# Kernel tuning notes

Measured on AMD Instinct MI355X. Metric: run time of the kernel, lower is better.

Reference implementation:

```python
import jax, jax.numpy as jnp
import numpy as np

N_NODES = 50000
N_EDGES = 800000
IN_FEAT = 64
HIDDEN = 128
NUM_LAYERS = 3


def setup_inputs() -> dict:
    key = jax.random.key(0)
    ks = jax.random.split(key, 8)
    x = jax.random.normal(ks[0], (N_NODES, IN_FEAT), dtype=jnp.float32)
    edge_index = jax.random.randint(ks[1], (2, N_EDGES), 0, N_NODES, dtype=jnp.int64)
    s_in = 1.0 / np.sqrt(IN_FEAT)
    s_h = 1.0 / np.sqrt(HIDDEN)
    W_in = jax.random.uniform(ks[2], (IN_FEAT, HIDDEN), jnp.float32, -s_in, s_in)
    b_in = jax.random.uniform(ks[3], (HIDDEN,), jnp.float32, -s_in, s_in)
    W_self = jax.random.uniform(ks[4], (NUM_LAYERS, HIDDEN, HIDDEN), jnp.float32, -s_h, s_h)
    b_self = jax.random.uniform(ks[5], (NUM_LAYERS, HIDDEN), jnp.float32, -s_h, s_h)
    W_nbr = jax.random.uniform(ks[6], (NUM_LAYERS, HIDDEN, HIDDEN), jnp.float32, -s_h, s_h)
    return {"x": x, "edge_index": edge_index, "W_in": W_in, "b_in": b_in,
            "W_self": W_self, "b_self": b_self, "W_nbr": W_nbr}


def reference(x, edge_index, W_in, b_in, W_self, b_self, W_nbr):
    # input projection: h [N, HIDDEN]
    h = x @ W_in + b_in
    src = edge_index[0]
    dst = edge_index[1]
    n = h.shape[0]
    ones = jnp.ones((dst.shape[0], 1), dtype=h.dtype)
    # scatter-mean denominator is grad-constant; compute once
    cnt = jax.ops.segment_sum(ones, dst, num_segments=n)
    cnt = jnp.maximum(cnt, 1.0)
    for l in range(W_self.shape[0]):
        msg = h[src] @ W_nbr[l]                               # [E, HIDDEN]
        agg = jax.ops.segment_sum(msg, dst, num_segments=n) / cnt  # scatter-mean
        h = jax.nn.elu(h @ W_self[l] + b_self[l] + agg)
    return h
```

## Files before the change

kernel.cpp:

```cpp
#include <hip/hip_runtime.h>
#include <cstdint>

#define HIDDEN 128

typedef unsigned short u16;
using frag_t  = __attribute__((ext_vector_type(8))) short;
using f32x4_t = __attribute__((ext_vector_type(4))) float;

__device__ __forceinline__ float bf2f(u16 u) {
    union { unsigned int i; float f; } c;
    c.i = ((unsigned int)u) << 16;
    return c.f;
}
__device__ __forceinline__ u16 f2bf(float f) {
    unsigned int u = __float_as_uint(f);
    unsigned int r = (u + 0x7fffu + ((u >> 16) & 1u)) >> 16;
    return (u16)r;
}

__device__ __forceinline__ size_t fmaj(int row, int col, int KF) {
    int T = row >> 4, m = row & 15;
    int f = col >> 5, q = (col & 31) >> 3, j = col & 7;
    return ((size_t)(T * KF + f) * 64 + q * 16 + m) * 8 + j;
}


__global__ void k_hist(const int* __restrict__ ei, int E, int* __restrict__ deg, int npr) {
    int r  = blockIdx.x & 7;
    int lo = r * npr, hi = lo + npr;
    int nb = gridDim.x >> 3;
    int bi = blockIdx.x >> 3;
    int tid = bi * blockDim.x + threadIdx.x;
    int stride = nb * blockDim.x;
    if ((E & 3) == 0) {
        const int4* d4 = (const int4*)(ei + E);
        int nch = E >> 2;
        for (int c = tid; c < nch; c += stride) {
            int4 d = d4[c];
            if (d.x >= lo && d.x < hi) atomicAdd(&deg[d.x], 1);
            if (d.y >= lo && d.y < hi) atomicAdd(&deg[d.y], 1);
            if (d.z >= lo && d.z < hi) atomicAdd(&deg[d.z], 1);
            if (d.w >= lo && d.w < hi) atomicAdd(&deg[d.w], 1);
        }
    } else {
        for (int e = tid; e < E; e += stride) {
            int d = ei[E + e];
            if (d >= lo && d < hi) atomicAdd(&deg[d], 1);
        }
    }
}

__global__ void k_scan1(const int* __restrict__ deg, int* __restrict__ rowp,
                        int* __restrict__ bsums, int n) {
    __shared__ int sh[1024];
    int t = threadIdx.x;
    int base = blockIdx.x * 1024;
    int v = (base + t < n) ? deg[base + t] : 0;
    sh[t] = v;
    __syncthreads();
    for (int off = 1; off < 1024; off <<= 1) {
        int x = sh[t];
        int y = (t >= off) ? sh[t - off] : 0;
        __syncthreads();
        sh[t] = x + y;
        __syncthreads();
    }
    if (base + t < n) rowp[base + t + 1] = sh[t];
    if (t == 1023) bsums[blockIdx.x] = sh[1023];
}

__global__ void k_scan2(int* __restrict__ bsums, int nb) {
    if (threadIdx.x == 0 && blockIdx.x == 0) {
        int run = 0;
        for (int b = 0; b < nb; ++b) { int v = bsums[b]; bsums[b] = run; run += v; }
    }
}

__global__ void k_scan3(int* __restrict__ rowp, const int* __restrict__ boffs,
                        int* __restrict__ fillp, int n) {
    int t = threadIdx.x;
    int b = blockIdx.x;
    int base = b * 1024;
    if (base + t < n) {
        int v = rowp[base + t + 1] + boffs[b];
        rowp[base + t + 1] = v;
        if (base + t + 1 < n) fillp[base + t + 1] = v;
    }
    if (b == 0 && t == 0) { rowp[0] = 0; fillp[0] = 0; }
}

__global__ void k_fill(const int* __restrict__ ei, int E,
                       int* __restrict__ fillpos, int* __restrict__ colx, int npr) {
    int r  = blockIdx.x & 7;
    int lo = r * npr, hi = lo + npr;
    int nb = gridDim.x >> 3;
    int bi = blockIdx.x >> 3;
    int tid = bi * blockDim.x + threadIdx.x;
    int stride = nb * blockDim.x;
    if ((E & 3) == 0) {
        const int4* s4 = (const int4*)ei;
        const int4* d4 = (const int4*)(ei + E);
        int nch = E >> 2;
        for (int c = tid; c < nch; c += stride) {
            int4 d = d4[c];
            bool m0 = d.x >= lo && d.x < hi;
            bool m1 = d.y >= lo && d.y < hi;
            bool m2 = d.z >= lo && d.z < hi;
            bool m3 = d.w >= lo && d.w < hi;
            if (m0 | m1 | m2 | m3) {
                int4 s = s4[c];
                if (m0) colx[atomicAdd(&fillpos[d.x], 1)] = s.x;
                if (m1) colx[atomicAdd(&fillpos[d.y], 1)] = s.y;
                if (m2) colx[atomicAdd(&fillpos[d.z], 1)] = s.z;
                if (m3) colx[atomicAdd(&fillpos[d.w], 1)] = s.w;
            }
        }
    } else {
        for (int e = tid; e < E; e += stride) {
            int d = ei[E + e];
            if (d >= lo && d < hi) colx[atomicAdd(&fillpos[d], 1)] = ei[e];
        }
    }
}


__global__ void k_prep_w(const float* __restrict__ W_in,
                         const float* __restrict__ W_self,
                         const float* __restrict__ W_nbr,
                         u16* __restrict__ WtI_hi, u16* __restrict__ WtI_lo,
                         u16* __restrict__ WtS_hi, u16* __restrict__ WtS_lo,
                         u16* __restrict__ WtN_hi, u16* __restrict__ WtN_lo,
                         int L) {
    int idx = blockIdx.x * blockDim.x + threadIdx.x;
    int nIn = 64 * 128;
    int nSq = L * 128 * 128;
    float v; u16* phi; u16* plo; int o;
    if (idx < nIn) {
        int n = idx / 64, k = idx % 64;
        v = W_in[k * 128 + n]; phi = WtI_hi; plo = WtI_lo; o = n * 64 + k;
    } else if (idx < nIn + nSq) {
        int t = idx - nIn;
        int l = t / (128 * 128), r = t % (128 * 128);
        int n = r / 128, k = r % 128;
        v = W_self[l * 128 * 128 + k * 128 + n]; phi = WtS_hi; plo = WtS_lo;
        o = l * 128 * 128 + n * 128 + k;
    } else if (idx < nIn + 2 * nSq) {
        int t = idx - nIn - nSq;
        int l = t / (128 * 128), r = t % (128 * 128);
        int n = r / 128, k = r % 128;
        v = W_nbr[l * 128 * 128 + k * 128 + n]; phi = WtN_hi; plo = WtN_lo;
        o = l * 128 * 128 + n * 128 + k;
    } else return;
    u16 hi = f2bf(v);
    phi[o] = hi;
    plo[o] = f2bf(v - bf2f(hi));
}

__global__ void k_prep_x(const float* __restrict__ x, u16* __restrict__ xf, int total) {
    int i = blockIdx.x * blockDim.x + threadIdx.x;
    int stride = gridDim.x * blockDim.x;
    for (; i < total; i += stride) {
        int row = i >> 6, col = i & 63;
        xf[fmaj(row, col, 2)] = f2bf(x[i]);
    }
}


__global__ void k_agg(const ushort4* __restrict__ hb4, const int* __restrict__ rowp,
                      const int* __restrict__ colx, u16* __restrict__ Sf, int n) {
    int g = (blockIdx.x * blockDim.x + threadIdx.x) >> 5;
    int lane = threadIdx.x & 31;
    if (g >= n) return;
    int beg = rowp[g];
    int end = rowp[g + 1];
    float4 a0 = make_float4(0.f, 0.f, 0.f, 0.f);
    float4 a1 = a0, a2 = a0, a3 = a0;
    int e = beg;
    for (; e + 7 < end; e += 8) {
        int s0 = colx[e],     s1 = colx[e + 1], s2 = colx[e + 2], s3 = colx[e + 3];
        int s4 = colx[e + 4], s5 = colx[e + 5], s6 = colx[e + 6], s7 = colx[e + 7];
        ushort4 v0 = hb4[(size_t)s0 * 32 + lane];
        ushort4 v1 = hb4[(size_t)s1 * 32 + lane];
        ushort4 v2 = hb4[(size_t)s2 * 32 + lane];
        ushort4 v3 = hb4[(size_t)s3 * 32 + lane];
        ushort4 v4 = hb4[(size_t)s4 * 32 + lane];
        ushort4 v5 = hb4[(size_t)s5 * 32 + lane];
        ushort4 v6 = hb4[(size_t)s6 * 32 + lane];
        ushort4 v7 = hb4[(size_t)s7 * 32 + lane];
        a0.x += bf2f(v0.x); a0.y += bf2f(v0.y); a0.z += bf2f(v0.z); a0.w += bf2f(v0.w);
        a1.x += bf2f(v1.x); a1.y += bf2f(v1.y); a1.z += bf2f(v1.z); a1.w += bf2f(v1.w);
        a2.x += bf2f(v2.x); a2.y += bf2f(v2.y); a2.z += bf2f(v2.z); a2.w += bf2f(v2.w);
        a3.x += bf2f(v3.x); a3.y += bf2f(v3.y); a3.z += bf2f(v3.z); a3.w += bf2f(v3.w);
        a0.x += bf2f(v4.x); a0.y += bf2f(v4.y); a0.z += bf2f(v4.z); a0.w += bf2f(v4.w);
        a1.x += bf2f(v5.x); a1.y += bf2f(v5.y); a1.z += bf2f(v5.z); a1.w += bf2f(v5.w);
        a2.x += bf2f(v6.x); a2.y += bf2f(v6.y); a2.z += bf2f(v6.z); a2.w += bf2f(v6.w);
        a3.x += bf2f(v7.x); a3.y += bf2f(v7.y); a3.z += bf2f(v7.z); a3.w += bf2f(v7.w);
    }
    for (; e + 3 < end; e += 4) {
        int s0 = colx[e], s1 = colx[e + 1], s2 = colx[e + 2], s3 = colx[e + 3];
        ushort4 v0 = hb4[(size_t)s0 * 32 + lane];
        ushort4 v1 = hb4[(size_t)s1 * 32 + lane];
        ushort4 v2 = hb4[(size_t)s2 * 32 + lane];
        ushort4 v3 = hb4[(size_t)s3 * 32 + lane];
        a0.x += bf2f(v0.x); a0.y += bf2f(v0.y); a0.z += bf2f(v0.z); a0.w += bf2f(v0.w);
        a1.x += bf2f(v1.x); a1.y += bf2f(v1.y); a1.z += bf2f(v1.z); a1.w += bf2f(v1.w);
        a2.x += bf2f(v2.x); a2.y += bf2f(v2.y); a2.z += bf2f(v2.z); a2.w += bf2f(v2.w);
        a3.x += bf2f(v3.x); a3.y += bf2f(v3.y); a3.z += bf2f(v3.z); a3.w += bf2f(v3.w);
    }
    for (; e < end; ++e) {
        int s = colx[e];
        ushort4 v = hb4[(size_t)s * 32 + lane];
        a0.x += bf2f(v.x); a0.y += bf2f(v.y); a0.z += bf2f(v.z); a0.w += bf2f(v.w);
    }
    float acc[4];
    acc[0] = (a0.x + a1.x) + (a2.x + a3.x);
    acc[1] = (a0.y + a1.y) + (a2.y + a3.y);
    acc[2] = (a0.z + a1.z) + (a2.z + a3.z);
    acc[3] = (a0.w + a1.w) + (a2.w + a3.w);
    int deg = end - beg;
    float inv = 1.0f / (float)(deg > 1 ? deg : 1);
    ushort4 ohi;
    u16* ph = &ohi.x;
#pragma unroll
    for (int c = 0; c < 4; ++c) ph[c] = f2bf(acc[c] * inv);
    int T = g >> 4, m = g & 15;
    int f = lane >> 3;
    int q = (lane & 7) >> 1;
    int jo = (lane & 1) * 4;
    *(ushort4*)&Sf[((size_t)(T * 4 + f) * 64 + q * 16 + m) * 8 + jo] = ohi;
}


template <int KF1, int KF2>
__global__ __launch_bounds__(256, 2) void k_gemm_mfma(
    const u16* __restrict__ A1f, const u16* __restrict__ A2f,
    const u16* __restrict__ B1h, const u16* __restrict__ B1l,
    const u16* __restrict__ B2h, const u16* __restrict__ B2l,
    const float* __restrict__ bias, float* __restrict__ C,
    u16* __restrict__ Hrow, u16* __restrict__ Hf,
    int M, int do_elu)
{
    constexpr int K1 = KF1 * 32;
    constexpr int K2 = KF2 * 32;
    constexpr int KF = KF1 + KF2;
    int lane = threadIdx.x & 63;
    int w    = threadIdx.x >> 6;
    int m16  = lane & 15;
    int quad = lane >> 4;
    int kq   = quad * 8;
    int ng   = (blockIdx.x >> 3) & 1;
    int mtb  = (blockIdx.x & 7) | ((blockIdx.x >> 4) << 3);
    int ncol = (ng * 4 + w) * 16 + m16;

    frag_t bh[KF], bl[KF];
    if (KF1) {
#pragma unroll
        for (int f = 0; f < KF1; ++f) {
            bh[f] = *(const frag_t*)&B1h[(size_t)ncol * K1 + f * 32 + kq];
            bl[f] = *(const frag_t*)&B1l[(size_t)ncol * K1 + f * 32 + kq];
        }
    }
    if (KF2) {
#pragma unroll
        for (int f = 0; f < KF2; ++f) {
            bh[KF1 + f] = *(const frag_t*)&B2h[(size_t)ncol * K2 + f * 32 + kq];
            bl[KF1 + f] = *(const frag_t*)&B2l[(size_t)ncol * K2 + f * 32 + kq];
        }
    }

    float bv = bias[ncol];
    int nMT  = (M + 31) >> 5;
    int step = gridDim.x >> 1;
    int fcol = ncol >> 5;
    int qcol = (ncol & 31) >> 3;
    int jcol = ncol & 7;

    for (int mt = mtb; mt < nMT; mt += step) {
        int T0 = mt * 2, T1 = T0 + 1;

        frag_t a0[KF], a1[KF];
        if (KF1) {
#pragma unroll
            for (int f = 0; f < KF1; ++f) {
                a0[f] = *(const frag_t*)&A1f[((size_t)(T0 * KF1 + f) * 64 + lane) * 8];
                a1[f] = *(const frag_t*)&A1f[((size_t)(T1 * KF1 + f) * 64 + lane) * 8];
            }
        }
        if (KF2) {
#pragma unroll
            for (int f = 0; f < KF2; ++f) {
                a0[KF1 + f] = *(const frag_t*)&A2f[((size_t)(T0 * KF2 + f) * 64 + lane) * 8];
                a1[KF1 + f] = *(const frag_t*)&A2f[((size_t)(T1 * KF2 + f) * 64 + lane) * 8];
            }
        }

        f32x4_t acc0 = (f32x4_t){0.f, 0.f, 0.f, 0.f};
        f32x4_t acc1 = (f32x4_t){0.f, 0.f, 0.f, 0.f};
#pragma unroll
        for (int f = 0; f < KF; ++f) {
            acc0 = __builtin_amdgcn_mfma_f32_16x16x32_bf16(a0[f], bh[f], acc0, 0, 0, 0);
            acc1 = __builtin_amdgcn_mfma_f32_16x16x32_bf16(a1[f], bh[f], acc1, 0, 0, 0);
            acc0 = __builtin_amdgcn_mfma_f32_16x16x32_bf16(a0[f], bl[f], acc0, 0, 0, 0);
            acc1 = __builtin_amdgcn_mfma_f32_16x16x32_bf16(a1[f], bl[f], acc1, 0, 0, 0);
        }

        int rb = mt * 32 + quad * 4;
#pragma unroll
        for (int r = 0; r < 4; ++r) {
#pragma unroll
            for (int half = 0; half < 2; ++half) {
                int row = rb + r + half * 16;
                float av = half ? acc1[r] : acc0[r];
                if (row < M) {
                    float v = av + bv;
                    if (do_elu) v = (v > 0.f) ? v : expm1f(v);
                    if (C) C[(size_t)row * HIDDEN + ncol] = v;
                    if (Hrow) {
                        u16 hv = f2bf(v);
                        Hrow[(size_t)row * HIDDEN + ncol] = hv;
                        Hf[((size_t)((row >> 4) * 4 + fcol) * 64 + qcol * 16 + (row & 15)) * 8 + jcol] = hv;
                    }
                }
            }
        }
    }
}


extern "C" void kernel_launch(void* const* d_in, const int* in_sizes, int n_in,
                              void* d_out, int out_size, void* d_ws, size_t ws_size,
                              hipStream_t stream) {
    const float* x        = (const float*)d_in[0];
    const int* ei         = (const int*)d_in[1];
    const float* W_in     = (const float*)d_in[2];
    const float* b_in     = (const float*)d_in[3];
    const float* W_self   = (const float*)d_in[4];
    const float* b_self   = (const float*)d_in[5];
    const float* W_nbr    = (const float*)d_in[6];
    float* out = (float*)d_out;

    const int IN_FEAT = 64;
    int N = in_sizes[0] / IN_FEAT;
    int E = in_sizes[1] / 2;
    int L = in_sizes[4] / (HIDDEN * HIDDEN);

    char* ws = (char*)d_ws;
    size_t off = 0;
    auto alloc = [&](size_t bytes) -> void* {
        void* p = ws + off;
        off = (off + bytes + 255) & ~(size_t)255;
        return p;
    };

    int nT = ((N + 31) / 32) * 2;

    u16* hRowA = (u16*)alloc((size_t)N * HIDDEN * 2);
    u16* hRowB = (u16*)alloc((size_t)N * HIDDEN * 2);
    u16* hfA   = (u16*)alloc((size_t)nT * 4 * 64 * 8 * 2);
    u16* hfB   = (u16*)alloc((size_t)nT * 4 * 64 * 8 * 2);
    u16* xf    = (u16*)alloc((size_t)nT * 2 * 64 * 8 * 2);
    u16* Sf    = (u16*)alloc((size_t)nT * 4 * 64 * 8 * 2);
    u16* WtI_hi = (u16*)alloc(128 * 64 * 2);
    u16* WtI_lo = (u16*)alloc(128 * 64 * 2);
    u16* WtS_hi = (u16*)alloc((size_t)L * 128 * 128 * 2);
    u16* WtS_lo = (u16*)alloc((size_t)L * 128 * 128 * 2);
    u16* WtN_hi = (u16*)alloc((size_t)L * 128 * 128 * 2);
    u16* WtN_lo = (u16*)alloc((size_t)L * 128 * 128 * 2);
    int* deg   = (int*)alloc((size_t)N * sizeof(int));
    int* rowp  = (int*)alloc((size_t)(N + 1) * sizeof(int));
    int* fillp = (int*)alloc((size_t)N * sizeof(int));
    int* colx  = (int*)alloc((size_t)E * sizeof(int));
    int* bsums = (int*)alloc(256 * sizeof(int));

    int npr = (N + 7) / 8;

    hipMemsetAsync(deg, 0, (size_t)N * sizeof(int), stream);
    k_hist<<<2048, 256, 0, stream>>>(ei, E, deg, npr);
    int nb = (N + 1023) / 1024;
    k_scan1<<<nb, 1024, 0, stream>>>(deg, rowp, bsums, N);
    k_scan2<<<1, 64, 0, stream>>>(bsums, nb);
    k_scan3<<<nb, 1024, 0, stream>>>(rowp, bsums, fillp, N);
    k_fill<<<2048, 256, 0, stream>>>(ei, E, fillp, colx, npr);

    int wtot = 64 * 128 + 2 * L * 128 * 128;
    k_prep_w<<<(wtot + 255) / 256, 256, 0, stream>>>(W_in, W_self, W_nbr,
                                                     WtI_hi, WtI_lo, WtS_hi, WtS_lo,
                                                     WtN_hi, WtN_lo, L);
    k_prep_x<<<1024, 256, 0, stream>>>(x, xf, N * IN_FEAT);

    const int GB = 1536;

    k_gemm_mfma<2, 0><<<GB, 256, 0, stream>>>(
        xf, nullptr,
        WtI_hi, WtI_lo, nullptr, nullptr,
        b_in, nullptr, hRowA, hfA, N, 0);

    u16* curRow = hRowA; u16* curF = hfA;
    u16* nxtRow = hRowB; u16* nxtF = hfB;

    for (int l = 0; l < L; ++l) {
        k_agg<<<(N + 7) / 8, 256, 0, stream>>>((const ushort4*)curRow, rowp, colx, Sf, N);
        const u16* Wsh = WtS_hi + (size_t)l * 128 * 128;
        const u16* Wsl = WtS_lo + (size_t)l * 128 * 128;
        const u16* Wnh = WtN_hi + (size_t)l * 128 * 128;
        const u16* Wnl = WtN_lo + (size_t)l * 128 * 128;
        const float* bs = b_self + (size_t)l * HIDDEN;
        bool last = (l == L - 1);
        k_gemm_mfma<4, 4><<<GB, 256, 0, stream>>>(
            curF, Sf,
            Wsh, Wsl, Wnh, Wnl,
            bs, last ? out : nullptr,
            last ? nullptr : nxtRow, last ? nullptr : nxtF, N, 1);
        u16* tr = curRow; curRow = nxtRow; nxtRow = tr;
        u16* tf = curF;   curF = nxtF;     nxtF = tf;
    }
}
```

Before: 357.9 us.

## Widen gather loads, prefetch GEMM A tiles, fuse prep kernels, warp-scan block sums

Several independent changes land together. Aggregation now uses 16 lanes per node with 16-byte bf16 loads and two accumulator sets instead of 32 lanes with 8-byte loads. The MFMA GEMM double-buffers A-fragment loads across M tiles, makes ELU a compile-time flag, and drops the grid from 1536 to 1024 blocks. The weight and x preparation kernels merge into one launch with vectorised x conversion, and the serial block-sum scan becomes a wavefront shuffle scan. The goals are fewer memory transactions in the gather, hidden load latency in the GEMM and less launch overhead, at the cost of more registers from double buffering and possibly lower occupancy.

New measurement: 338.9 us. 5.3% less time.

```diff
diff --git a/kernel.cpp b/kernel.cpp
--- a/kernel.cpp
+++ b/kernel.cpp
@@ -4,8 +4,9 @@
 #define HIDDEN 128
 
 typedef unsigned short u16;
-using frag_t  = __attribute__((ext_vector_type(8))) short;
-using f32x4_t = __attribute__((ext_vector_type(4))) float;
+using frag_t   = __attribute__((ext_vector_type(8))) short;
+using f32x4_t  = __attribute__((ext_vector_type(4))) float;
+using ushort8_t = __attribute__((ext_vector_type(8))) unsigned short;
 
 __device__ __forceinline__ float bf2f(u16 u) {
     union { unsigned int i; float f; } c;
@@ -70,9 +71,19 @@
 }
 
 __global__ void k_scan2(int* __restrict__ bsums, int nb) {
-    if (threadIdx.x == 0 && blockIdx.x == 0) {
-        int run = 0;
-        for (int b = 0; b < nb; ++b) { int v = bsums[b]; bsums[b] = run; run += v; }
+    int lane = threadIdx.x;
+    int carry = 0;
+    for (int base = 0; base < nb; base += 64) {
+        int i = base + lane;
+        int v = (i < nb) ? bsums[i] : 0;
+        int incl = v;
+#pragma unroll
+        for (int off = 1; off < 64; off <<= 1) {
+            int y = __shfl_up(incl, off, 64);
+            if (lane >= off) incl += y;
+        }
+        if (i < nb) bsums[i] = carry + (incl - v);
+        carry += __shfl(incl, 63, 64);
     }
 }
 
@@ -124,121 +135,125 @@
 }
 
 
-__global__ void k_prep_w(const float* __restrict__ W_in,
-                         const float* __restrict__ W_self,
-                         const float* __restrict__ W_nbr,
-                         u16* __restrict__ WtI_hi, u16* __restrict__ WtI_lo,
-                         u16* __restrict__ WtS_hi, u16* __restrict__ WtS_lo,
-                         u16* __restrict__ WtN_hi, u16* __restrict__ WtN_lo,
-                         int L) {
-    int idx = blockIdx.x * blockDim.x + threadIdx.x;
+__global__ void k_prep(const float* __restrict__ x,
+                       const float* __restrict__ W_in,
+                       const float* __restrict__ W_self,
+                       const float* __restrict__ W_nbr,
+                       u16* __restrict__ xf,
+                       u16* __restrict__ WtI_hi, u16* __restrict__ WtI_lo,
+                       u16* __restrict__ WtS_hi, u16* __restrict__ WtS_lo,
+                       u16* __restrict__ WtN_hi, u16* __restrict__ WtN_lo,
+                       int L, int nxg) {
     int nIn = 64 * 128;
     int nSq = L * 128 * 128;
-    float v; u16* phi; u16* plo; int o;
-    if (idx < nIn) {
-        int n = idx / 64, k = idx % 64;
-        v = W_in[k * 128 + n]; phi = WtI_hi; plo = WtI_lo; o = n * 64 + k;
-    } else if (idx < nIn + nSq) {
-        int t = idx - nIn;
-        int l = t / (128 * 128), r = t % (128 * 128);
-        int n = r / 128, k = r % 128;
-        v = W_self[l * 128 * 128 + k * 128 + n]; phi = WtS_hi; plo = WtS_lo;
-        o = l * 128 * 128 + n * 128 + k;
-    } else if (idx < nIn + 2 * nSq) {
-        int t = idx - nIn - nSq;
-        int l = t / (128 * 128), r = t % (128 * 128);
-        int n = r / 128, k = r % 128;
-        v = W_nbr[l * 128 * 128 + k * 128 + n]; phi = WtN_hi; plo = WtN_lo;
-        o = l * 128 * 128 + n * 128 + k;
-    } else return;
-    u16 hi = f2bf(v);
-    phi[o] = hi;
-    plo[o] = f2bf(v - bf2f(hi));
-}
-
-__global__ void k_prep_x(const float* __restrict__ x, u16* __restrict__ xf, int total) {
-    int i = blockIdx.x * blockDim.x + threadIdx.x;
+    int wtot = nIn + 2 * nSq;
+    int total = wtot + nxg;
     int stride = gridDim.x * blockDim.x;
-    for (; i < total; i += stride) {
-        int row = i >> 6, col = i & 63;
-        xf[fmaj(row, col, 2)] = f2bf(x[i]);
-    }
-}
-
-
-__global__ void k_agg(const ushort4* __restrict__ hb4, const int* __restrict__ rowp,
-                      const int* __restrict__ colx, u16* __restrict__ Sf, int n) {
-    int g = (blockIdx.x * blockDim.x + threadIdx.x) >> 5;
-    int lane = threadIdx.x & 31;
+    for (int i = blockIdx.x * blockDim.x + threadIdx.x; i < total; i += stride) {
+        if (i >= wtot) {
+            int t = i - wtot;
+            int row = t >> 3, c = t & 7;
+            const float4* xs = (const float4*)(x + (size_t)row * 64 + c * 8);
+            float4 v0 = xs[0], v1 = xs[1];
+            ushort8_t o;
+            o[0] = f2bf(v0.x); o[1] = f2bf(v0.y); o[2] = f2bf(v0.z); o[3] = f2bf(v0.w);
+            o[4] = f2bf(v1.x); o[5] = f2bf(v1.y); o[6] = f2bf(v1.z); o[7] = f2bf(v1.w);
+            int T = row >> 4, m = row & 15;
+            int f = c >> 2, q = c & 3;
+            *(ushort8_t*)&xf[((size_t)(T * 2 + f) * 64 + q * 16 + m) * 8] = o;
+        } else {
+            float v; u16* phi; u16* plo; int o;
+            if (i < nIn) {
+                int n = i / 64, k = i % 64;
+                v = W_in[k * 128 + n]; phi = WtI_hi; plo = WtI_lo; o = n * 64 + k;
+            } else if (i < nIn + nSq) {
+                int t = i - nIn;
+                int l = t / (128 * 128), r = t % (128 * 128);
+                int n = r / 128, k = r % 128;
+                v = W_self[l * 128 * 128 + k * 128 + n]; phi = WtS_hi; plo = WtS_lo;
+                o = l * 128 * 128 + n * 128 + k;
+            } else {
+                int t = i - nIn - nSq;
+                int l = t / (128 * 128), r = t % (128 * 128);
+                int n = r / 128, k = r % 128;
+                v = W_nbr[l * 128 * 128 + k * 128 + n]; phi = WtN_hi; plo = WtN_lo;
+                o = l * 128 * 128 + n * 128 + k;
+            }
+            u16 hi = f2bf(v);
+            phi[o] = hi;
+            plo[o] = f2bf(v - bf2f(hi));
+        }
+    }
+}
+
+
+__global__ __launch_bounds__(256, 4) void k_agg(
+        const ushort8_t* __restrict__ hb8, const int* __restrict__ rowp,
+        const int* __restrict__ colx, u16* __restrict__ Sf, int n) {
+    int g = (blockIdx.x * blockDim.x + threadIdx.x) >> 4;
+    int lane = threadIdx.x & 15;
     if (g >= n) return;
     int beg = rowp[g];
     int end = rowp[g + 1];
-    float4 a0 = make_float4(0.f, 0.f, 0.f, 0.f);
-    float4 a1 = a0, a2 = a0, a3 = a0;
+    float a0[8], a1[8];
+#pragma unroll
+    for (int j = 0; j < 8; ++j) { a0[j] = 0.f; a1[j] = 0.f; }
     int e = beg;
     for (; e + 7 < end; e += 8) {
         int s0 = colx[e],     s1 = colx[e + 1], s2 = colx[e + 2], s3 = colx[e + 3];
         int s4 = colx[e + 4], s5 = colx[e + 5], s6 = colx[e + 6], s7 = colx[e + 7];
-        ushort4 v0 = hb4[(size_t)s0 * 32 + lane];
-        ushort4 v1 = hb4[(size_t)s1 * 32 + lane];
-        ushort4 v2 = hb4[(size_t)s2 * 32 + lane];
-        ushort4 v3 = hb4[(size_t)s3 * 32 + lane];
-        ushort4 v4 = hb4[(size_t)s4 * 32 + lane];
-        ushort4 v5 = hb4[(size_t)s5 * 32 + lane];
-        ushort4 v6 = hb4[(size_t)s6 * 32 + lane];
-        ushort4 v7 = hb4[(size_t)s7 * 32 + lane];
-        a0.x += bf2f(v0.x); a0.y += bf2f(v0.y); a0.z += bf2f(v0.z); a0.w += bf2f(v0.w);
-        a1.x += bf2f(v1.x); a1.y += bf2f(v1.y); a1.z += bf2f(v1.z); a1.w += bf2f(v1.w);
-        a2.x += bf2f(v2.x); a2.y += bf2f(v2.y); a2.z += bf2f(v2.z); a2.w += bf2f(v2.w);
-        a3.x += bf2f(v3.x); a3.y += bf2f(v3.y); a3.z += bf2f(v3.z); a3.w += bf2f(v3.w);
-        a0.x += bf2f(v4.x); a0.y += bf2f(v4.y); a0.z += bf2f(v4.z); a0.w += bf2f(v4.w);
-        a1.x += bf2f(v5.x); a1.y += bf2f(v5.y); a1.z += bf2f(v5.z); a1.w += bf2f(v5.w);
-        a2.x += bf2f(v6.x); a2.y += bf2f(v6.y); a2.z += bf2f(v6.z); a2.w += bf2f(v6.w);
-        a3.x += bf2f(v7.x); a3.y += bf2f(v7.y); a3.z += bf2f(v7.z); a3.w += bf2f(v7.w);
+        ushort8_t v0 = hb8[(size_t)s0 * 16 + lane];
+        ushort8_t v1 = hb8[(size_t)s1 * 16 + lane];
+        ushort8_t v2 = hb8[(size_t)s2 * 16 + lane];
+        ushort8_t v3 = hb8[(size_t)s3 * 16 + lane];
+        ushort8_t v4 = hb8[(size_t)s4 * 16 + lane];
+        ushort8_t v5 = hb8[(size_t)s5 * 16 + lane];
+        ushort8_t v6 = hb8[(size_t)s6 * 16 + lane];
+        ushort8_t v7 = hb8[(size_t)s7 * 16 + lane];
+#pragma unroll
+        for (int j = 0; j < 8; ++j) {
+            a0[j] += bf2f(v0[j]); a1[j] += bf2f(v1[j]);
+            a0[j] += bf2f(v2[j]); a1[j] += bf2f(v3[j]);
+            a0[j] += bf2f(v4[j]); a1[j] += bf2f(v5[j]);
+            a0[j] += bf2f(v6[j]); a1[j] += bf2f(v7[j]);
+        }
     }
     for (; e + 3 < end; e += 4) {
         int s0 = colx[e], s1 = colx[e + 1], s2 = colx[e + 2], s3 = colx[e + 3];
-        ushort4 v0 = hb4[(size_t)s0 * 32 + lane];
-        ushort4 v1 = hb4[(size_t)s1 * 32 + lane];
-        ushort4 v2 = hb4[(size_t)s2 * 32 + lane];
-        ushort4 v3 = hb4[(size_t)s3 * 32 + lane];
-        a0.x += bf2f(v0.x); a0.y += bf2f(v0.y); a0.z += bf2f(v0.z); a0.w += bf2f(v0.w);
-        a1.x += bf2f(v1.x); a1.y += bf2f(v1.y); a1.z += bf2f(v1.z); a1.w += bf2f(v1.w);
-        a2.x += bf2f(v2.x); a2.y += bf2f(v2.y); a2.z += bf2f(v2.z); a2.w += bf2f(v2.w);
-        a3.x += bf2f(v3.x); a3.y += bf2f(v3.y); a3.z += bf2f(v3.z); a3.w += bf2f(v3.w);
+        ushort8_t v0 = hb8[(size_t)s0 * 16 + lane];
+        ushort8_t v1 = hb8[(size_t)s1 * 16 + lane];
+        ushort8_t v2 = hb8[(size_t)s2 * 16 + lane];
+        ushort8_t v3 = hb8[(size_t)s3 * 16 + lane];
+#pragma unroll
+        for (int j = 0; j < 8; ++j) {
+            a0[j] += bf2f(v0[j]); a1[j] += bf2f(v1[j]);
+            a0[j] += bf2f(v2[j]); a1[j] += bf2f(v3[j]);
+        }
     }
     for (; e < end; ++e) {
         int s = colx[e];
-        ushort4 v = hb4[(size_t)s * 32 + lane];
-        a0.x += bf2f(v.x); a0.y += bf2f(v.y); a0.z += bf2f(v.z); a0.w += bf2f(v.w);
-    }
-    float acc[4];
-    acc[0] = (a0.x + a1.x) + (a2.x + a3.x);
-    acc[1] = (a0.y + a1.y) + (a2.y + a3.y);
-    acc[2] = (a0.z + a1.z) + (a2.z + a3.z);
-    acc[3] = (a0.w + a1.w) + (a2.w + a3.w);
+        ushort8_t v = hb8[(size_t)s * 16 + lane];
+#pragma unroll
+        for (int j = 0; j < 8; ++j) a0[j] += bf2f(v[j]);
+    }
     int deg = end - beg;
     float inv = 1.0f / (float)(deg > 1 ? deg : 1);
-    ushort4 ohi;
-    u16* ph = &ohi.x;
-#pragma unroll
-    for (int c = 0; c < 4; ++c) ph[c] = f2bf(acc[c] * inv);
+    ushort8_t o;
+#pragma unroll
+    for (int j = 0; j < 8; ++j) o[j] = f2bf((a0[j] + a1[j]) * inv);
     int T = g >> 4, m = g & 15;
-    int f = lane >> 3;
-    int q = (lane & 7) >> 1;
-    int jo = (lane & 1) * 4;
-    *(ushort4*)&Sf[((size_t)(T * 4 + f) * 64 + q * 16 + m) * 8 + jo] = ohi;
-}
-
-
-template <int KF1, int KF2>
+    *(ushort8_t*)&Sf[((size_t)(T * 4 + (lane >> 2)) * 64 + (lane & 3) * 16 + m) * 8] = o;
+}
+
+
+template <int KF1, int KF2, int DO_ELU>
 __global__ __launch_bounds__(256, 2) void k_gemm_mfma(
     const u16* __restrict__ A1f, const u16* __restrict__ A2f,
     const u16* __restrict__ B1h, const u16* __restrict__ B1l,
     const u16* __restrict__ B2h, const u16* __restrict__ B2l,
     const float* __restrict__ bias, float* __restrict__ C,
     u16* __restrict__ Hrow, u16* __restrict__ Hf,
-    int M, int do_elu)
+    int M)
 {
     constexpr int K1 = KF1 * 32;
     constexpr int K2 = KF2 * 32;
@@ -253,14 +268,14 @@
     int ncol = (ng * 4 + w) * 16 + m16;
 
     frag_t bh[KF], bl[KF];
-    if (KF1) {
+    if constexpr (KF1 > 0) {
 #pragma unroll
         for (int f = 0; f < KF1; ++f) {
             bh[f] = *(const frag_t*)&B1h[(size_t)ncol * K1 + f * 32 + kq];
             bl[f] = *(const frag_t*)&B1l[(size_t)ncol * K1 + f * 32 + kq];
         }
     }
-    if (KF2) {
+    if constexpr (KF2 > 0) {
 #pragma unroll
         for (int f = 0; f < KF2; ++f) {
             bh[KF1 + f] = *(const frag_t*)&B2h[(size_t)ncol * K2 + f * 32 + kq];
@@ -275,25 +290,25 @@
     int qcol = (ncol & 31) >> 3;
     int jcol = ncol & 7;
 
-    for (int mt = mtb; mt < nMT; mt += step) {
+    auto loadA = [&](int mt, frag_t (&a0)[KF], frag_t (&a1)[KF]) {
         int T0 = mt * 2, T1 = T0 + 1;
-
-        frag_t a0[KF], a1[KF];
-        if (KF1) {
+        if constexpr (KF1 > 0) {
 #pragma unroll
             for (int f = 0; f < KF1; ++f) {
                 a0[f] = *(const frag_t*)&A1f[((size_t)(T0 * KF1 + f) * 64 + lane) * 8];
                 a1[f] = *(const frag_t*)&A1f[((size_t)(T1 * KF1 + f) * 64 + lane) * 8];
             }
         }
-        if (KF2) {
+        if constexpr (KF2 > 0) {
 #pragma unroll
             for (int f = 0; f < KF2; ++f) {
                 a0[KF1 + f] = *(const frag_t*)&A2f[((size_t)(T0 * KF2 + f) * 64 + lane) * 8];
                 a1[KF1 + f] = *(const frag_t*)&A2f[((size_t)(T1 * KF2 + f) * 64 + lane) * 8];
             }
         }
-
+    };
+
+    auto compute = [&](int mt, frag_t (&a0)[KF], frag_t (&a1)[KF]) {
         f32x4_t acc0 = (f32x4_t){0.f, 0.f, 0.f, 0.f};
         f32x4_t acc1 = (f32x4_t){0.f, 0.f, 0.f, 0.f};
 #pragma unroll
@@ -303,7 +318,6 @@
             acc0 = __builtin_amdgcn_mfma_f32_16x16x32_bf16(a0[f], bl[f], acc0, 0, 0, 0);
             acc1 = __builtin_amdgcn_mfma_f32_16x16x32_bf16(a1[f], bl[f], acc1, 0, 0, 0);
         }
-
         int rb = mt * 32 + quad * 4;
 #pragma unroll
         for (int r = 0; r < 4; ++r) {
@@ -313,7 +327,7 @@
                 float av = half ? acc1[r] : acc0[r];
                 if (row < M) {
                     float v = av + bv;
-                    if (do_elu) v = (v > 0.f) ? v : expm1f(v);
+                    if constexpr (DO_ELU) v = (v > 0.f) ? v : expm1f(v);
                     if (C) C[(size_t)row * HIDDEN + ncol] = v;
                     if (Hrow) {
                         u16 hv = f2bf(v);
@@ -323,6 +337,22 @@
                 }
             }
         }
+    };
+
+    int mt = mtb;
+    if (mt >= nMT) return;
+    frag_t xa0[KF], xa1[KF], ya0[KF], ya1[KF];
+    loadA(mt, xa0, xa1);
+    while (true) {
+        int mt2 = mt + step;
+        if (mt2 < nMT) loadA(mt2, ya0, ya1);
+        compute(mt, xa0, xa1);
+        if (mt2 >= nMT) break;
+        int mt3 = mt2 + step;
+        if (mt3 < nMT) loadA(mt3, xa0, xa1);
+        compute(mt2, ya0, ya1);
+        if (mt3 >= nMT) break;
+        mt = mt3;
     }
 }
 
@@ -383,34 +413,34 @@
     k_fill<<<2048, 256, 0, stream>>>(ei, E, fillp, colx, npr);
 
     int wtot = 64 * 128 + 2 * L * 128 * 128;
-    k_prep_w<<<(wtot + 255) / 256, 256, 0, stream>>>(W_in, W_self, W_nbr,
-                                                     WtI_hi, WtI_lo, WtS_hi, WtS_lo,
-                                                     WtN_hi, WtN_lo, L);
-    k_prep_x<<<1024, 256, 0, stream>>>(x, xf, N * IN_FEAT);
-
-    const int GB = 1536;
-
-    k_gemm_mfma<2, 0><<<GB, 256, 0, stream>>>(
+    int prep_total = wtot + N * 8;
+    k_prep<<<(prep_total + 255) / 256, 256, 0, stream>>>(
+        x, W_in, W_self, W_nbr, xf,
+        WtI_hi, WtI_lo, WtS_hi, WtS_lo, WtN_hi, WtN_lo, L, N * 8);
+
+    const int GB = 1024;
+
+    k_gemm_mfma<2, 0, 0><<<GB, 256, 0, stream>>>(
         xf, nullptr,
         WtI_hi, WtI_lo, nullptr, nullptr,
-        b_in, nullptr, hRowA, hfA, N, 0);
+        b_in, nullptr, hRowA, hfA, N);
 
     u16* curRow = hRowA; u16* curF = hfA;
     u16* nxtRow = hRowB; u16* nxtF = hfB;
 
     for (int l = 0; l < L; ++l) {
-        k_agg<<<(N + 7) / 8, 256, 0, stream>>>((const ushort4*)curRow, rowp, colx, Sf, N);
+        k_agg<<<(N + 15) / 16, 256, 0, stream>>>((const ushort8_t*)curRow, rowp, colx, Sf, N);
         const u16* Wsh = WtS_hi + (size_t)l * 128 * 128;
         const u16* Wsl = WtS_lo + (size_t)l * 128 * 128;
         const u16* Wnh = WtN_hi + (size_t)l * 128 * 128;
         const u16* Wnl = WtN_lo + (size_t)l * 128 * 128;
         const float* bs = b_self + (size_t)l * HIDDEN;
         bool last = (l == L - 1);
-        k_gemm_mfma<4, 4><<<GB, 256, 0, stream>>>(
+        k_gemm_mfma<4, 4, 1><<<GB, 256, 0, stream>>>(
             curF, Sf,
             Wsh, Wsl, Wnh, Wnl,
             bs, last ? out : nullptr,
-            last ? nullptr : nxtRow, last ? nullptr : nxtF, N, 1);
+            last ? nullptr : nxtRow, last ? nullptr : nxtF, N);
         u16* tr = curRow; curRow = nxtRow; nxtRow = tr;
         u16* tf = curF;   curF = nxtF;     nxtF = tf;
     }
```
